# Optimization experiments

Hardware: AMD Instinct MI355X
Metric: run time of the kernel (lower is better)

Reference implementation:

```python
import jax, jax.numpy as jnp
import numpy as np

N = 102400       # total nodes (1024 graphs x 100 nodes)
E = 1638400      # edges (avg degree 16)
B = 1024         # graphs; also GRU sequence length (unbatched 2D GRU input)
F_IN, HID, H1 = 4, 16, 6
OUT, FC1, RNN, ACT = 32, 64, 64, 11


def _gat(x, src, dst, W, a_src, a_dst, b, heads, out_dim, concat):
    # PyG GATConv (eval mode, dropout off), add_self_loops=True
    n = x.shape[0]
    loop = jnp.arange(n, dtype=src.dtype)
    s = jnp.concatenate([src, loop])
    d = jnp.concatenate([dst, loop])
    h = (x @ W.T).reshape(n, heads, out_dim)                 # [N,H,F]
    a_s = (h * a_src).sum(-1)                                # [N,H]
    a_d = (h * a_dst).sum(-1)                                # [N,H]
    e = jax.nn.leaky_relu(a_s[s] + a_d[d], 0.2)              # [E',H]
    m = jax.ops.segment_max(e, d, num_segments=n)
    p = jnp.exp(e - m[d])
    alpha = p / jax.ops.segment_sum(p, d, num_segments=n)[d]
    agg = jax.ops.segment_sum(h[s] * alpha[:, :, None], d, num_segments=n)  # [N,H,F]
    agg = agg.reshape(n, heads * out_dim) if concat else agg.mean(axis=1)
    return agg + b


def _gru(xs, wih, whh, bih, bhh):
    # torch nn.GRU, unbatched: xs is [L, FC1], h0 = zeros
    def step(hp, xt):
        gi = xt @ wih.T + bih
        gh = hp @ whh.T + bhh
        ir, iz, i_n = jnp.split(gi, 3)
        hr, hz, h_n = jnp.split(gh, 3)
        r = jax.nn.sigmoid(ir + hr)
        z = jax.nn.sigmoid(iz + hz)
        ng = jnp.tanh(i_n + r * h_n)
        h = (1.0 - z) * ng + z * hp
        return h, h
    _, ys = jax.lax.scan(step, jnp.zeros((RNN,), xs.dtype), xs)
    return ys


def setup_inputs():
    key = jax.random.key(0)
    ks = jax.random.split(key, 16)
    g = lambda i, shape, fan: jax.random.normal(ks[i], shape, jnp.float32) / np.sqrt(fan)
    x = jax.random.normal(ks[0], (N, F_IN), jnp.float32)
    src = jax.random.randint(ks[1], (E,), 0, N)
    dst = jax.random.randint(ks[2], (E,), 0, N)
    dst = jnp.where(dst == src, (dst + 1) % N, dst)  # no pre-existing self-loops
    edge_index = jnp.stack([src, dst]).astype(jnp.int32)
    robot_index = (jnp.arange(B) * (N // B)).astype(jnp.int32)  # ptr[:-1]
    robot_features = jax.random.normal(ks[3], (B, 4), jnp.float32)
    return dict(
        x=x, edge_index=edge_index, robot_index=robot_index, robot_features=robot_features,
        c1_W=g(4, (H1 * HID, F_IN), F_IN), c1_as=g(5, (H1, HID), HID), c1_ad=g(6, (H1, HID), HID),
        c1_b=jnp.zeros((H1 * HID,), jnp.float32),
        c2_W=g(7, (OUT, H1 * HID), H1 * HID), c2_as=g(8, (1, OUT), OUT), c2_ad=g(9, (1, OUT), OUT),
        c2_b=jnp.zeros((OUT,), jnp.float32),
        fc1_W=g(10, (FC1, OUT + 4), OUT + 4), fc1_b=jnp.zeros((FC1,), jnp.float32),
        gru_wih=g(11, (3 * RNN, FC1), FC1), gru_whh=g(12, (3 * RNN, RNN), RNN),
        gru_bih=jnp.zeros((3 * RNN,), jnp.float32), gru_bhh=jnp.zeros((3 * RNN,), jnp.float32),
        fc2_W=g(13, (ACT, RNN), RNN), fc2_b=jnp.zeros((ACT,), jnp.float32),
    )


def reference(x, edge_index, robot_index, robot_features,
              c1_W, c1_as, c1_ad, c1_b, c2_W, c2_as, c2_ad, c2_b,
              fc1_W, fc1_b, gru_wih, gru_whh, gru_bih, gru_bhh, fc2_W, fc2_b):
    src, dst = edge_index[0], edge_index[1]
    h = _gat(x, src, dst, c1_W, c1_as, c1_ad, c1_b, H1, HID, True)   # [N, 96]
    h = jnp.tanh(h)
    h = _gat(h, src, dst, c2_W, c2_as, c2_ad, c2_b, 1, OUT, False)   # [N, 32]
    h = h[robot_index]                                               # [B, 32]
    h = jnp.tanh(jnp.concatenate([h, robot_features], axis=1) @ fc1_W.T + fc1_b)  # [B, 64]
    h = _gru(h, gru_wih, gru_whh, gru_bih, gru_bhh)                  # [B, 64]
    return h @ fc2_W.T + fc2_b                                       # [B, 11] logits
```

## Files before the change

kernel.cpp:

```cpp
#include <hip/hip_runtime.h>

#define S2CAP 24576
#define DEG   96
#define CH    16

typedef float f32x4 __attribute__((ext_vector_type(4)));

__device__ __forceinline__ float fsig(float x){ return 1.f/(1.f + __expf(-x)); }
__device__ __forceinline__ float ftanh(float a){
  a = fminf(fmaxf(a, -15.f), 15.f);
  float e2 = __expf(2.f*a);
  return (e2 - 1.f)/(e2 + 1.f);
}
__device__ __forceinline__ float attw(float e){
  e = (e > 0.f) ? e : 0.2f*e;
  return __expf(e);
}

__global__ void k_init(const float* __restrict__ c1W, const float* __restrict__ c1as,
                       const float* __restrict__ c1ad, float* __restrict__ AsAd,
                       const int* __restrict__ rix, int B, int* __restrict__ sidx,
                       int* __restrict__ nodeof, int* __restrict__ ctrl,
                       int* __restrict__ cnt1){
  int gid = blockIdx.x*blockDim.x + threadIdx.x;
  if (gid == 0) ctrl[0] = B;
  if (gid < 48){
    int which = gid/24, r = gid%24, k = r/6, h = r%6;
    const float* av = which ? c1ad : c1as;
    float s = 0.f;
    for (int f = 0; f < 16; ++f) s += c1W[(h*16+f)*4 + k] * av[h*16+f];
    AsAd[which*24 + k*6 + h] = s;
  }
  if (gid < B){ int r = rix[gid]; sidx[r] = gid; nodeof[gid] = r; }
  if (gid < S2CAP) cnt1[gid] = 0;
}

__global__ void k_claim(const int* __restrict__ ei, int E, int B,
                        int* __restrict__ sidx, int* __restrict__ nodeof,
                        int* __restrict__ ctrl){
  int e = blockIdx.x*blockDim.x + threadIdx.x;
  if (e >= E) return;
  int d = ei[E + e];
  int sd = sidx[d];
  if (sd < 0 || sd >= B) return;
  int s = ei[e];
  if (sidx[s] < 0){
    int old = atomicCAS(&sidx[s], -1, -2);
    if (old == -1){
      int id = atomicAdd(&ctrl[0], 1);
      if (id < S2CAP){ nodeof[id] = s; sidx[s] = id; }
      else sidx[s] = -1;
    }
  }
}

__global__ void k_scat(const int* __restrict__ ei, int E,
                       const int* __restrict__ sidx, int* __restrict__ cnt1,
                       int* __restrict__ csr1){
  int e = blockIdx.x*blockDim.x + threadIdx.x;
  if (e >= E) return;
  int sd = sidx[ei[E + e]];
  if (sd >= 0){
    int p = atomicAdd(&cnt1[sd], 1);
    if (p < DEG) csr1[sd*DEG + p] = ei[e];
  }
}

__global__ void k_gat1(const float* __restrict__ x, const float* __restrict__ c1W,
                       const float* __restrict__ c1b, const float* __restrict__ AsAd,
                       const int* __restrict__ nodeof, const int* __restrict__ cnt1,
                       const int* __restrict__ csr1, const int* __restrict__ ctrl,
                       float* __restrict__ tbuf){
  int gid = blockIdx.x*blockDim.x + threadIdx.x;
  int sid = gid/6, h = gid - sid*6;
  if (sid >= ctrl[0]) return;
  float Ask[4], Adk[4];
  #pragma unroll
  for (int k = 0; k < 4; ++k){ Ask[k] = AsAd[k*6+h]; Adk[k] = AsAd[24 + k*6 + h]; }
  float W[16][4];
  #pragma unroll
  for (int f = 0; f < 16; ++f)
    #pragma unroll
    for (int k = 0; k < 4; ++k) W[f][k] = c1W[(h*16+f)*4 + k];
  int d = nodeof[sid];
  float4 xd = *(const float4*)(x + 4*(size_t)d);
  float ad = xd.x*Adk[0] + xd.y*Adk[1] + xd.z*Adk[2] + xd.w*Adk[3];
  int beg = sid*DEG, n = cnt1[sid];
  n = (n < DEG) ? n : DEG;
  float den = 0.f, agg[16];
  #pragma unroll
  for (int f = 0; f < 16; ++f) agg[f] = 0.f;
  for (int j = -1; j < n; ++j){
    int s = (j < 0) ? d : csr1[beg + j];
    float4 xv = *(const float4*)(x + 4*(size_t)s);
    float as = xv.x*Ask[0] + xv.y*Ask[1] + xv.z*Ask[2] + xv.w*Ask[3];
    float wgt = attw(as + ad);
    den += wgt;
    #pragma unroll
    for (int f = 0; f < 16; ++f){
      float h1 = xv.x*W[f][0] + xv.y*W[f][1] + xv.z*W[f][2] + xv.w*W[f][3];
      agg[f] = fmaf(wgt, h1, agg[f]);
    }
  }
  float inv = 1.f/den;
  #pragma unroll
  for (int f = 0; f < 16; ++f)
    tbuf[(size_t)sid*96 + h*16 + f] = ftanh(agg[f]*inv + c1b[h*16+f]);
}

__global__ void k_h2att(const float* __restrict__ c2W, const float* __restrict__ tbuf,
                        const float* __restrict__ c2as, const float* __restrict__ c2ad,
                        const int* __restrict__ ctrl, float* __restrict__ h2,
                        float* __restrict__ as2, float* __restrict__ ad2){
  int gid = blockIdx.x*blockDim.x + threadIdx.x;
  int sid = gid >> 5, o = gid & 31;
  bool act = sid < ctrl[0];
  float s = 0.f;
  if (act){
    const float* t = tbuf + (size_t)sid*96;
    const float* wr = c2W + o*96;
    #pragma unroll
    for (int j = 0; j < 96; ++j) s = fmaf(wr[j], t[j], s);
    h2[(size_t)sid*32 + o] = s;
  }
  float a = act ? s*c2as[o] : 0.f;
  float b = act ? s*c2ad[o] : 0.f;
  #pragma unroll
  for (int w = 16; w >= 1; w >>= 1){
    a += __shfl_xor(a, w, 32);
    b += __shfl_xor(b, w, 32);
  }
  if (act && o == 0){ as2[sid] = a; ad2[sid] = b; }
}

__global__ void k_gat2fc1(const float* __restrict__ h2, const float* __restrict__ as2,
                          const float* __restrict__ ad2, const float* __restrict__ c2b,
                          const float* __restrict__ rf, const float* __restrict__ fc1W,
                          const float* __restrict__ fc1b, const int* __restrict__ sidx,
                          const int* __restrict__ cnt1, const int* __restrict__ csr1,
                          float* __restrict__ xs, int B){
  int rp = blockIdx.x*blockDim.x + threadIdx.x;
  if (rp >= B) return;
  float ad = ad2[rp];
  float den = 0.f, agg[32];
  #pragma unroll
  for (int o = 0; o < 32; ++o) agg[o] = 0.f;
  int beg = rp*DEG, n = cnt1[rp];
  n = (n < DEG) ? n : DEG;
  for (int j = -1; j < n; ++j){
    int ss;
    if (j < 0) ss = rp;
    else { int s = csr1[beg + j]; ss = sidx[s]; if (ss < 0 || ss >= S2CAP) continue; }
    float wgt = attw(as2[ss] + ad);
    den += wgt;
    const float* hv = h2 + (size_t)ss*32;
    #pragma unroll
    for (int o = 0; o < 32; ++o) agg[o] = fmaf(wgt, hv[o], agg[o]);
  }
  float inv = 1.f/den;
  float cat[36];
  #pragma unroll
  for (int o = 0; o < 32; ++o) cat[o] = agg[o]*inv + c2b[o];
  #pragma unroll
  for (int k = 0; k < 4; ++k) cat[32+k] = rf[rp*4+k];
  for (int o = 0; o < 64; ++o){
    float s = fc1b[o];
    const float* wrow = fc1W + o*36;
    #pragma unroll
    for (int j = 0; j < 36; ++j) s = fmaf(wrow[j], cat[j], s);
    xs[(size_t)rp*64 + o] = ftanh(s);
  }
}

__global__ void k_gi(const float* __restrict__ xs, const float* __restrict__ wih,
                     const float* __restrict__ bih, const float* __restrict__ bhh,
                     float* __restrict__ gi, int B){
  int gid = blockIdx.x*blockDim.x + threadIdx.x;
  if (gid >= B*192) return;
  int t = gid/192, g = gid - t*192;
  const float* xv = xs + (size_t)t*64;
  const float* wr = wih + (size_t)g*64;
  float s = bih[g] + (g < 128 ? bhh[g] : 0.f);
  #pragma unroll
  for (int k = 0; k < 64; ++k) s = fmaf(wr[k], xv[k], s);
  gi[gid] = s;
}

__global__ __launch_bounds__(192, 1) void k_gru3(const float* __restrict__ gi,
                       const float* __restrict__ whh, const float* __restrict__ bhh,
                       float* __restrict__ ys, int B){
  int tid = threadIdx.x;
  int w = tid >> 6, u = tid & 63, g = tid;
  const float* p = whh + (size_t)g*64;
  f32x4 w0,w1,w2,w3,w4,w5,w6,w7,w8,w9,w10,w11,w12,w13,w14,w15;
#define LDW(R, OFF) asm volatile("global_load_dwordx4 %0, %1, off offset:" #OFF : "=v"(R) : "v"(p))
  LDW(w0,0);    LDW(w1,16);   LDW(w2,32);   LDW(w3,48);
  LDW(w4,64);   LDW(w5,80);   LDW(w6,96);   LDW(w7,112);
  LDW(w8,128);  LDW(w9,144);  LDW(w10,160); LDW(w11,176);
  LDW(w12,192); LDW(w13,208); LDW(w14,224); LDW(w15,240);
#undef LDW
  asm volatile("s_waitcnt vmcnt(0)" ::: "memory");
  __builtin_amdgcn_sched_barrier(0);
  float bb = (w == 2) ? bhh[128 + u] : 0.f;

  __shared__ float gbuf[3][CH*192];
  __shared__ float rzbuf[2][256];
  int nch = (B + CH - 1)/CH;

  auto stage = [&](int cbuf, int chunk){
    if (chunk >= nch) return;
    const float* gb = gi + (size_t)chunk*(CH*192) + w*1024 + u*4;
    float* lb = &gbuf[cbuf][w*1024];
    __builtin_amdgcn_global_load_lds(
      (const __attribute__((address_space(1))) unsigned int*)(gb),
      (__attribute__((address_space(3))) unsigned int*)(lb), 16, 0, 0);
    __builtin_amdgcn_global_load_lds(
      (const __attribute__((address_space(1))) unsigned int*)(gb + 256),
      (__attribute__((address_space(3))) unsigned int*)(lb + 256), 16, 0, 0);
    __builtin_amdgcn_global_load_lds(
      (const __attribute__((address_space(1))) unsigned int*)(gb + 512),
      (__attribute__((address_space(3))) unsigned int*)(lb + 512), 16, 0, 0);
    __builtin_amdgcn_global_load_lds(
      (const __attribute__((address_space(1))) unsigned int*)(gb + 768),
      (__attribute__((address_space(3))) unsigned int*)(lb + 768), 16, 0, 0);
  };

  stage(0, 0);
  stage(1, 1);

  float hvec = 0.f, gcur = 0.f;
#define PIN(R) asm volatile("" : "+v"(R))
#define DOT4(W, K)                                                    \
  { float h0_ = __int_as_float(__builtin_amdgcn_readlane(hb, (K)));   \
    float h1_ = __int_as_float(__builtin_amdgcn_readlane(hb, (K)+1)); \
    float h2_ = __int_as_float(__builtin_amdgcn_readlane(hb, (K)+2)); \
    float h3_ = __int_as_float(__builtin_amdgcn_readlane(hb, (K)+3)); \
    a0 = fmaf(W.x, h0_, a0); a1 = fmaf(W.y, h1_, a1);                 \
    a2 = fmaf(W.z, h2_, a2); a3 = fmaf(W.w, h3_, a3); }

  int cbx = 0;
  for (int c = 0; c < nch; ++c){
    int nbx = cbx + 1; if (nbx == 3) nbx = 0;
    int sbx = nbx + 1; if (sbx == 3) sbx = 0;
    asm volatile("s_waitcnt vmcnt(0)" ::: "memory");
    __syncthreads();
    stage(sbx, c + 2);
    if (c == 0) gcur = gbuf[0][g];
    int lim = B - c*CH; if (lim > CH) lim = CH;
    for (int ti = 0; ti < lim; ++ti){
      int t = c*CH + ti;
      PIN(w0); PIN(w1); PIN(w2);  PIN(w3);  PIN(w4);  PIN(w5);  PIN(w6);  PIN(w7);
      PIN(w8); PIN(w9); PIN(w10); PIN(w11); PIN(w12); PIN(w13); PIN(w14); PIN(w15);
      float gnext = (ti + 1 < CH) ? gbuf[cbx][(ti+1)*192 + g] : gbuf[nbx][g];
      float a0 = 0.f, a1 = 0.f, a2 = 0.f, a3 = 0.f;
      int hb = __float_as_int(hvec);
      DOT4(w0,0);   DOT4(w1,4);   DOT4(w2,8);   DOT4(w3,12);
      DOT4(w4,16);  DOT4(w5,20);  DOT4(w6,24);  DOT4(w7,28);
      DOT4(w8,32);  DOT4(w9,36);  DOT4(w10,40); DOT4(w11,44);
      DOT4(w12,48); DOT4(w13,52); DOT4(w14,56); DOT4(w15,60);
      float dot = (a0 + a1) + (a2 + a3);
      float* buf = rzbuf[t & 1];
      if (w < 2){
        buf[w*64 + u] = gcur + dot;
      } else {
        buf[128 + u] = dot + bb;
        buf[192 + u] = gcur;
      }
      __syncthreads();
      float pre_r = buf[u], pre_z = buf[64 + u], an = buf[128 + u], i_n = buf[192 + u];
      float r  = fsig(pre_r);
      float z  = fsig(pre_z);
      float ng = ftanh(i_n + r*an);
      float hnew = (1.f - z)*ng + z*hvec;
      if (w == 2) ys[(size_t)t*64 + u] = hnew;
      hvec = hnew;
      gcur = gnext;
    }
    cbx = nbx;
  }
#undef PIN
#undef DOT4
}

__global__ void k_fc2(const float* __restrict__ ys, const float* __restrict__ f2W,
                      const float* __restrict__ f2b, float* __restrict__ out, int B){
  int gid = blockIdx.x*blockDim.x + threadIdx.x;
  if (gid >= B*11) return;
  int t = gid/11, a = gid - t*11;
  const float* hv = ys + (size_t)t*64;
  const float* wr = f2W + a*64;
  float s = f2b[a];
  #pragma unroll
  for (int k = 0; k < 64; ++k) s = fmaf(wr[k], hv[k], s);
  out[gid] = s;
}

extern "C" void kernel_launch(void* const* d_in, const int* in_sizes, int n_in,
                              void* d_out, int out_size, void* d_ws, size_t ws_size,
                              hipStream_t stream) {
  (void)n_in; (void)out_size; (void)ws_size;
  const float* x    = (const float*)d_in[0];
  const int*   ei   = (const int*)d_in[1];
  const int*   rix  = (const int*)d_in[2];
  const float* rf   = (const float*)d_in[3];
  const float* c1W  = (const float*)d_in[4];
  const float* c1as = (const float*)d_in[5];
  const float* c1ad = (const float*)d_in[6];
  const float* c1b  = (const float*)d_in[7];
  const float* c2W  = (const float*)d_in[8];
  const float* c2as = (const float*)d_in[9];
  const float* c2ad = (const float*)d_in[10];
  const float* c2b  = (const float*)d_in[11];
  const float* fc1W = (const float*)d_in[12];
  const float* fc1b = (const float*)d_in[13];
  const float* wih  = (const float*)d_in[14];
  const float* whh  = (const float*)d_in[15];
  const float* bih  = (const float*)d_in[16];
  const float* bhh  = (const float*)d_in[17];
  const float* f2W  = (const float*)d_in[18];
  const float* f2b  = (const float*)d_in[19];
  float* out = (float*)d_out;

  const int N = in_sizes[0]/4;
  const int E = in_sizes[1]/2;
  const int B = in_sizes[2];

  char* w = (char*)d_ws;
  size_t off = 0;
  auto take = [&](size_t bytes)->char*{
    char* p = w + off;
    off = (off + bytes + 255) & ~(size_t)255;
    return p;
  };
  int*   ctrl   = (int*)  take(256);
  float* AsAd   = (float*)take(256);
  int*   sidx   = (int*)  take((size_t)N*4);
  int*   nodeof = (int*)  take((size_t)S2CAP*4);
  int*   cnt1   = (int*)  take((size_t)S2CAP*4);
  int*   csr1   = (int*)  take((size_t)S2CAP*DEG*4);
  float* tbuf   = (float*)take((size_t)S2CAP*96*4);
  float* h2     = (float*)take((size_t)S2CAP*32*4);
  float* as2    = (float*)take((size_t)S2CAP*4);
  float* ad2    = (float*)take((size_t)S2CAP*4);
  float* xs     = (float*)take((size_t)B*64*4);
  float* gi     = (float*)take((size_t)B*192*4);
  float* ys     = (float*)take((size_t)B*64*4);

  hipMemsetAsync(sidx, 0xFF, (size_t)N*4, stream);

  k_init   <<<(S2CAP+255)/256, 256, 0, stream>>>(c1W, c1as, c1ad, AsAd, rix, B, sidx, nodeof, ctrl, cnt1);
  k_claim  <<<(E+255)/256, 256, 0, stream>>>(ei, E, B, sidx, nodeof, ctrl);
  k_scat   <<<(E+255)/256, 256, 0, stream>>>(ei, E, sidx, cnt1, csr1);
  k_gat1   <<<(S2CAP*6+255)/256, 256, 0, stream>>>(x, c1W, c1b, AsAd, nodeof, cnt1, csr1, ctrl, tbuf);
  k_h2att  <<<(S2CAP*32+255)/256, 256, 0, stream>>>(c2W, tbuf, c2as, c2ad, ctrl, h2, as2, ad2);
  k_gat2fc1<<<(B+255)/256, 256, 0, stream>>>(h2, as2, ad2, c2b, rf, fc1W, fc1b, sidx, cnt1, csr1, xs, B);
  k_gi     <<<(B*192+255)/256, 256, 0, stream>>>(xs, wih, bih, bhh, gi, B);
  k_gru3   <<<1, 192, 0, stream>>>(gi, whh, bhh, ys, B);
  k_fc2    <<<(B*11+255)/256, 256, 0, stream>>>(ys, f2W, f2b, out, B);
}
```

Baseline: 931.4 us.

## Fuse GAT2, FC1 and GRU input projection; fold FC2 into GRU kernel

```diff
diff --git a/kernel.cpp b/kernel.cpp
--- a/kernel.cpp
+++ b/kernel.cpp
@@ -133,62 +133,84 @@
   if (act && o == 0){ as2[sid] = a; ad2[sid] = b; }
 }
 
-__global__ void k_gat2fc1(const float* __restrict__ h2, const float* __restrict__ as2,
-                          const float* __restrict__ ad2, const float* __restrict__ c2b,
-                          const float* __restrict__ rf, const float* __restrict__ fc1W,
-                          const float* __restrict__ fc1b, const int* __restrict__ sidx,
-                          const int* __restrict__ cnt1, const int* __restrict__ csr1,
-                          float* __restrict__ xs, int B){
-  int rp = blockIdx.x*blockDim.x + threadIdx.x;
-  if (rp >= B) return;
+__global__ __launch_bounds__(192) void k_g2g(const float* __restrict__ h2,
+                        const float* __restrict__ as2, const float* __restrict__ ad2,
+                        const float* __restrict__ c2b, const float* __restrict__ rf,
+                        const float* __restrict__ fc1W, const float* __restrict__ fc1b,
+                        const int* __restrict__ sidx, const int* __restrict__ cnt1,
+                        const int* __restrict__ csr1, const float* __restrict__ wih,
+                        const float* __restrict__ bih, const float* __restrict__ bhh,
+                        float* __restrict__ gi){
+  int rp = blockIdx.x, tid = threadIdx.x;
+  __shared__ float cat[36];
+  __shared__ float xsl[64];
   float ad = ad2[rp];
-  float den = 0.f, agg[32];
-  #pragma unroll
-  for (int o = 0; o < 32; ++o) agg[o] = 0.f;
   int beg = rp*DEG, n = cnt1[rp];
   n = (n < DEG) ? n : DEG;
-  for (int j = -1; j < n; ++j){
-    int ss;
-    if (j < 0) ss = rp;
-    else { int s = csr1[beg + j]; ss = sidx[s]; if (ss < 0 || ss >= S2CAP) continue; }
-    float wgt = attw(as2[ss] + ad);
-    den += wgt;
-    const float* hv = h2 + (size_t)ss*32;
-    #pragma unroll
-    for (int o = 0; o < 32; ++o) agg[o] = fmaf(wgt, hv[o], agg[o]);
-  }
-  float inv = 1.f/den;
-  float cat[36];
-  #pragma unroll
-  for (int o = 0; o < 32; ++o) cat[o] = agg[o]*inv + c2b[o];
-  #pragma unroll
-  for (int k = 0; k < 4; ++k) cat[32+k] = rf[rp*4+k];
-  for (int o = 0; o < 64; ++o){
-    float s = fc1b[o];
-    const float* wrow = fc1W + o*36;
+  if (tid < 32){
+    int o = tid;
+    float den = 0.f, agg = 0.f;
+    for (int j = -1; j < n; ++j){
+      int ss;
+      if (j < 0) ss = rp;
+      else { int s = csr1[beg + j]; ss = sidx[s]; if (ss < 0 || ss >= S2CAP) continue; }
+      float wgt = attw(as2[ss] + ad);
+      den += wgt;
+      agg = fmaf(wgt, h2[(size_t)ss*32 + o], agg);
+    }
+    cat[o] = agg/den + c2b[o];
+    if (o < 4) cat[32 + o] = rf[rp*4 + o];
+  }
+  __syncthreads();
+  if (tid < 64){
+    float s = fc1b[tid];
+    const float* wrow = fc1W + tid*36;
     #pragma unroll
     for (int j = 0; j < 36; ++j) s = fmaf(wrow[j], cat[j], s);
-    xs[(size_t)rp*64 + o] = ftanh(s);
-  }
-}
-
-__global__ void k_gi(const float* __restrict__ xs, const float* __restrict__ wih,
-                     const float* __restrict__ bih, const float* __restrict__ bhh,
-                     float* __restrict__ gi, int B){
-  int gid = blockIdx.x*blockDim.x + threadIdx.x;
-  if (gid >= B*192) return;
-  int t = gid/192, g = gid - t*192;
-  const float* xv = xs + (size_t)t*64;
-  const float* wr = wih + (size_t)g*64;
-  float s = bih[g] + (g < 128 ? bhh[g] : 0.f);
-  #pragma unroll
-  for (int k = 0; k < 64; ++k) s = fmaf(wr[k], xv[k], s);
-  gi[gid] = s;
-}
+    xsl[tid] = ftanh(s);
+  }
+  __syncthreads();
+  {
+    int g = tid;
+    const float* wr = wih + (size_t)g*64;
+    float s = bih[g] + (g < 128 ? bhh[g] : 0.f);
+    #pragma unroll
+    for (int k = 0; k < 64; ++k) s = fmaf(wr[k], xsl[k], s);
+    gi[(size_t)rp*192 + g] = s;
+  }
+}
+
+#define STEP8(WA, WB, L0,L1,L2,L3,L4,L5,L6,L7) do {                   \
+  int s0_,s1_,s2_,s3_,s4_,s5_,s6_,s7_;                                \
+  asm volatile(                                                       \
+    "v_readlane_b32 %0, %12, " #L0 "\n\t"                             \
+    "v_readlane_b32 %1, %12, " #L1 "\n\t"                             \
+    "v_readlane_b32 %2, %12, " #L2 "\n\t"                             \
+    "v_readlane_b32 %3, %12, " #L3 "\n\t"                             \
+    "v_readlane_b32 %4, %12, " #L4 "\n\t"                             \
+    "v_readlane_b32 %5, %12, " #L5 "\n\t"                             \
+    "v_readlane_b32 %6, %12, " #L6 "\n\t"                             \
+    "v_readlane_b32 %7, %12, " #L7 "\n\t"                             \
+    "v_fmac_f32 %8, %0, %13\n\t"                                      \
+    "v_fmac_f32 %9, %1, %14\n\t"                                      \
+    "v_fmac_f32 %10, %2, %15\n\t"                                     \
+    "v_fmac_f32 %11, %3, %16\n\t"                                     \
+    "v_fmac_f32 %8, %4, %17\n\t"                                      \
+    "v_fmac_f32 %9, %5, %18\n\t"                                      \
+    "v_fmac_f32 %10, %6, %19\n\t"                                     \
+    "v_fmac_f32 %11, %7, %20\n\t"                                     \
+    : "=&s"(s0_),"=&s"(s1_),"=&s"(s2_),"=&s"(s3_),                    \
+      "=&s"(s4_),"=&s"(s5_),"=&s"(s6_),"=&s"(s7_),                    \
+      "+v"(a0),"+v"(a1),"+v"(a2),"+v"(a3)                             \
+    : "v"(hvec),                                                      \
+      "v"(WA.x),"v"(WA.y),"v"(WA.z),"v"(WA.w),                        \
+      "v"(WB.x),"v"(WB.y),"v"(WB.z),"v"(WB.w));                       \
+} while(0)
 
 __global__ __launch_bounds__(192, 1) void k_gru3(const float* __restrict__ gi,
                        const float* __restrict__ whh, const float* __restrict__ bhh,
-                       float* __restrict__ ys, int B){
+                       float* __restrict__ ys, const float* __restrict__ f2W,
+                       const float* __restrict__ f2b, float* __restrict__ out, int B){
   int tid = threadIdx.x;
   int w = tid >> 6, u = tid & 63, g = tid;
   const float* p = whh + (size_t)g*64;
@@ -229,15 +251,6 @@
   stage(1, 1);
 
   float hvec = 0.f, gcur = 0.f;
-#define PIN(R) asm volatile("" : "+v"(R))
-#define DOT4(W, K)                                                    \
-  { float h0_ = __int_as_float(__builtin_amdgcn_readlane(hb, (K)));   \
-    float h1_ = __int_as_float(__builtin_amdgcn_readlane(hb, (K)+1)); \
-    float h2_ = __int_as_float(__builtin_amdgcn_readlane(hb, (K)+2)); \
-    float h3_ = __int_as_float(__builtin_amdgcn_readlane(hb, (K)+3)); \
-    a0 = fmaf(W.x, h0_, a0); a1 = fmaf(W.y, h1_, a1);                 \
-    a2 = fmaf(W.z, h2_, a2); a3 = fmaf(W.w, h3_, a3); }
-
   int cbx = 0;
   for (int c = 0; c < nch; ++c){
     int nbx = cbx + 1; if (nbx == 3) nbx = 0;
@@ -249,15 +262,16 @@
     int lim = B - c*CH; if (lim > CH) lim = CH;
     for (int ti = 0; ti < lim; ++ti){
       int t = c*CH + ti;
-      PIN(w0); PIN(w1); PIN(w2);  PIN(w3);  PIN(w4);  PIN(w5);  PIN(w6);  PIN(w7);
-      PIN(w8); PIN(w9); PIN(w10); PIN(w11); PIN(w12); PIN(w13); PIN(w14); PIN(w15);
       float gnext = (ti + 1 < CH) ? gbuf[cbx][(ti+1)*192 + g] : gbuf[nbx][g];
       float a0 = 0.f, a1 = 0.f, a2 = 0.f, a3 = 0.f;
-      int hb = __float_as_int(hvec);
-      DOT4(w0,0);   DOT4(w1,4);   DOT4(w2,8);   DOT4(w3,12);
-      DOT4(w4,16);  DOT4(w5,20);  DOT4(w6,24);  DOT4(w7,28);
-      DOT4(w8,32);  DOT4(w9,36);  DOT4(w10,40); DOT4(w11,44);
-      DOT4(w12,48); DOT4(w13,52); DOT4(w14,56); DOT4(w15,60);
+      STEP8(w0, w1,  0, 1, 2, 3, 4, 5, 6, 7);
+      STEP8(w2, w3,  8, 9,10,11,12,13,14,15);
+      STEP8(w4, w5, 16,17,18,19,20,21,22,23);
+      STEP8(w6, w7, 24,25,26,27,28,29,30,31);
+      STEP8(w8, w9, 32,33,34,35,36,37,38,39);
+      STEP8(w10,w11,40,41,42,43,44,45,46,47);
+      STEP8(w12,w13,48,49,50,51,52,53,54,55);
+      STEP8(w14,w15,56,57,58,59,60,61,62,63);
       float dot = (a0 + a1) + (a2 + a3);
       float* buf = rzbuf[t & 1];
       if (w < 2){
@@ -271,29 +285,26 @@
       float r  = fsig(pre_r);
       float z  = fsig(pre_z);
       float ng = ftanh(i_n + r*an);
-      float hnew = (1.f - z)*ng + z*hvec;
+      float hnew = ng + z*(hvec - ng);
       if (w == 2) ys[(size_t)t*64 + u] = hnew;
       hvec = hnew;
       gcur = gnext;
     }
     cbx = nbx;
   }
-#undef PIN
-#undef DOT4
-}
-
-__global__ void k_fc2(const float* __restrict__ ys, const float* __restrict__ f2W,
-                      const float* __restrict__ f2b, float* __restrict__ out, int B){
-  int gid = blockIdx.x*blockDim.x + threadIdx.x;
-  if (gid >= B*11) return;
-  int t = gid/11, a = gid - t*11;
-  const float* hv = ys + (size_t)t*64;
-  const float* wr = f2W + a*64;
-  float s = f2b[a];
-  #pragma unroll
-  for (int k = 0; k < 64; ++k) s = fmaf(wr[k], hv[k], s);
-  out[gid] = s;
-}
+  asm volatile("s_waitcnt vmcnt(0)" ::: "memory");
+  __syncthreads();
+  for (int idx = tid; idx < B*11; idx += 192){
+    int t = idx/11, a = idx - t*11;
+    const float* hv = ys + (size_t)t*64;
+    const float* wr = f2W + a*64;
+    float s = f2b[a];
+    #pragma unroll
+    for (int k = 0; k < 64; ++k) s = fmaf(wr[k], hv[k], s);
+    out[idx] = s;
+  }
+}
+#undef STEP8
 
 extern "C" void kernel_launch(void* const* d_in, const int* in_sizes, int n_in,
                               void* d_out, int out_size, void* d_ws, size_t ws_size,
@@ -342,7 +353,6 @@
   float* h2     = (float*)take((size_t)S2CAP*32*4);
   float* as2    = (float*)take((size_t)S2CAP*4);
   float* ad2    = (float*)take((size_t)S2CAP*4);
-  float* xs     = (float*)take((size_t)B*64*4);
   float* gi     = (float*)take((size_t)B*192*4);
   float* ys     = (float*)take((size_t)B*64*4);
 
@@ -353,8 +363,6 @@
   k_scat   <<<(E+255)/256, 256, 0, stream>>>(ei, E, sidx, cnt1, csr1);
   k_gat1   <<<(S2CAP*6+255)/256, 256, 0, stream>>>(x, c1W, c1b, AsAd, nodeof, cnt1, csr1, ctrl, tbuf);
   k_h2att  <<<(S2CAP*32+255)/256, 256, 0, stream>>>(c2W, tbuf, c2as, c2ad, ctrl, h2, as2, ad2);
-  k_gat2fc1<<<(B+255)/256, 256, 0, stream>>>(h2, as2, ad2, c2b, rf, fc1W, fc1b, sidx, cnt1, csr1, xs, B);
-  k_gi     <<<(B*192+255)/256, 256, 0, stream>>>(xs, wih, bih, bhh, gi, B);
-  k_gru3   <<<1, 192, 0, stream>>>(gi, whh, bhh, ys, B);
-  k_fc2    <<<(B*11+255)/256, 256, 0, stream>>>(ys, f2W, f2b, out, B);
-}
+  k_g2g    <<<B, 192, 0, stream>>>(h2, as2, ad2, c2b, rf, fc1W, fc1b, sidx, cnt1, csr1, wih, bih, bhh, gi);
+  k_gru3   <<<1, 192, 0, stream>>>(gi, whh, bhh, ys, f2W, f2b, out, B);
+}
```

Result: slower. 1.029 ms (+10.5%).
